# Performance work log

Hardware: AMD Instinct MI355X
Metric: run time of the kernel (lower is better)

## Reference

```python
import jax, jax.numpy as jnp
import numpy as np


def toeplitz_from(weight_matrix):
    # Faithful to the torch Toeplitz parametrization:
    # parameters = concat(W[::-1, 0], W[0, 1:]); toep[i, j] = parameters[n_rows-1-i+j]
    n_rows, n_cols = weight_matrix.shape
    params = jnp.concatenate([weight_matrix[::-1, 0], weight_matrix[0, 1:]])
    idx = (n_rows - 1) - jnp.arange(n_rows)[:, None] + jnp.arange(n_cols)[None, :]
    return params[idx]  # [n_rows, n_cols], built in one gather instead of a loop


def setup_inputs() -> dict:
    key = jax.random.key(0)
    ks = jax.random.split(key, 8)
    B, frame_dim, esn_dim, last_dim = 65536, 64, 960, 1024
    comb = frame_dim + esn_dim
    s1 = 1.0 / np.sqrt(comb)
    s2 = 1.0 / np.sqrt(last_dim)
    return {
        "x_frame": jax.random.normal(ks[0], (B, frame_dim), jnp.float32),
        "h_esn": jax.random.normal(ks[1], (B, esn_dim), jnp.float32),
        "W1": jax.random.normal(ks[2], (last_dim, comb), jnp.float32) * s1,
        "b1": jax.random.normal(ks[3], (last_dim,), jnp.float32) * s1,
        "W_slope": jax.random.normal(ks[4], (frame_dim, last_dim), jnp.float32) * s2,
        "b_slope": jax.random.normal(ks[5], (frame_dim,), jnp.float32) * s2,
        "W_int": jax.random.normal(ks[6], (frame_dim, last_dim), jnp.float32) * s2,
        "b_int": jax.random.normal(ks[7], (frame_dim,), jnp.float32) * s2,
    }


def reference(x_frame, h_esn, W1, b1, W_slope, b_slope, W_int, b_int):
    W1_toep = toeplitz_from(W1)                      # [last_dim, frame+esn]
    combined = jnp.concatenate([x_frame, h_esn], axis=-1)  # [B, frame+esn]
    q_last = jax.nn.relu(combined @ W1_toep.T + b1)  # [B, last_dim]
    slope = jnp.tanh(q_last @ W_slope.T + b_slope)   # [B, frame_dim]
    intercept = q_last @ W_int.T + b_int             # [B, frame_dim]
    return slope, intercept
```

## Files before the change

kernel.cpp:

```cpp
#include <hip/hip_runtime.h>
#include <cstdint>
#include <cstddef>

typedef __bf16 bf16x8v __attribute__((ext_vector_type(8)));
typedef float f32x4v __attribute__((ext_vector_type(4)));

__device__ __forceinline__ void gload_lds16(const void* g, void* l) {
  __builtin_amdgcn_global_load_lds((const __attribute__((address_space(1))) void*)g,
                                   (__attribute__((address_space(3))) void*)l,
                                   16, 0, 0);
}

__device__ __forceinline__ bf16x8v cvt_bf16x8(f32x4v a, f32x4v b) {
  bf16x8v r;
  r[0] = (__bf16)a[0]; r[1] = (__bf16)a[1]; r[2] = (__bf16)a[2]; r[3] = (__bf16)a[3];
  r[4] = (__bf16)b[0]; r[5] = (__bf16)b[1]; r[6] = (__bf16)b[2]; r[7] = (__bf16)b[3];
  return r;
}

__global__ __launch_bounds__(256) void prep_kernel(const float* __restrict__ W1,
                                                   const float* __restrict__ Wslope,
                                                   const float* __restrict__ Wint,
                                                   __bf16* __restrict__ toep,
                                                   __bf16* __restrict__ Wcat) {
  int id = blockIdx.x * 256 + threadIdx.x;
  if (id < 1024 * 1024) {
    int i = id >> 10, j = id & 1023;
    int p = 1023 - i + j;
    float v = (p < 1024) ? W1[(size_t)(1023 - p) << 10] : W1[p - 1023];
    toep[id] = (__bf16)v;
  } else {
    int id2 = id - 1024 * 1024;
    int n = id2 >> 10, k = id2 & 1023;
    float v = (n < 64) ? Wslope[((size_t)n << 10) + k] : Wint[((size_t)(n - 64) << 10) + k];
    Wcat[id2] = (__bf16)v;
  }
}

__global__ __launch_bounds__(256) void gemm1_f32dma(const float* __restrict__ x,
                                                    const float* __restrict__ h,
                                                    const __bf16* __restrict__ toep,
                                                    const float* __restrict__ b1,
                                                    __bf16* __restrict__ q) {
  __shared__ __align__(16) float  Af[2][128 * 32];
  __shared__ __align__(16) __bf16 Bf[2][128 * 32];
  const int tid = threadIdx.x, wid = tid >> 6, lane = tid & 63;
  const int wrow = wid >> 1, wcol = wid & 1;
  const int bid = blockIdx.x;
  const int xcd = bid & 7, j = bid >> 3;
  const int m0 = (((j >> 3) << 3) | xcd) << 7;
  const int n0 = (j & 7) << 7;
  const int quad = lane >> 4, l15 = lane & 15;
  const int rl8 = lane >> 3, s8 = lane & 7;
  const int sA = s8 ^ rl8;
  const int rl4 = lane >> 2, s4 = lane & 3;
  const int sB = s4 ^ (rl4 & 3);

  f32x4v acc[4][4] = {};

  const int arow = m0 + wid * 32;
  const __bf16* gB = toep + (((size_t)(n0 + wid * 32 + rl4)) << 10) + sB * 8;
  const size_t BROW16 = (size_t)16 << 10;

  auto stageA = [&](float* la, int kt) {
    const int k0 = kt << 5;
    const float* src;
    int rstride;
    if (k0 < 64) { src = x + (size_t)(arow + rl8) * 64 + k0 + sA * 4;        rstride = 8 * 64; }
    else         { src = h + (size_t)(arow + rl8) * 960 + (k0 - 64) + sA * 4; rstride = 8 * 960; }
    const int rb = wid * 32;
#pragma unroll
    for (int i = 0; i < 4; ++i) {
      gload_lds16(src, &la[(rb + i * 8) * 32]);
      src += rstride;
    }
  };
  auto stageB = [&](__bf16* lb) {
    const int rb = wid * 32;
    gload_lds16(gB,          &lb[rb * 32]);
    gload_lds16(gB + BROW16, &lb[(rb + 16) * 32]);
    gB += 32;
  };

  auto compute = [&](const float* la, const __bf16* lb) {
    bf16x8v af[4], bfr[4];
#pragma unroll
    for (int r = 0; r < 4; ++r) {
      const int row = wrow * 64 + r * 16 + l15;
      const f32x4v* base = (const f32x4v*)&la[row * 32];
      f32x4v lo = base[(quad * 2)     ^ (row & 7)];
      f32x4v hi = base[(quad * 2 + 1) ^ (row & 7)];
      af[r] = cvt_bf16x8(lo, hi);
    }
#pragma unroll
    for (int c = 0; c < 4; ++c) {
      const int row = wcol * 64 + c * 16 + l15;
      const bf16x8v* bb = (const bf16x8v*)&lb[row * 32];
      bfr[c] = bb[quad ^ (row & 3)];
    }
#pragma unroll
    for (int r = 0; r < 4; ++r)
#pragma unroll
      for (int c = 0; c < 4; ++c)
        acc[r][c] = __builtin_amdgcn_mfma_f32_16x16x32_bf16(af[r], bfr[c], acc[r][c], 0, 0, 0);
  };

  stageA(Af[0], 0); stageB(Bf[0]);
  for (int kt = 0; kt < 32; kt += 2) {
    __syncthreads();
    stageA(Af[1], kt + 1); stageB(Bf[1]);
    compute(Af[0], Bf[0]);
    __syncthreads();
    if (kt < 30) { stageA(Af[0], kt + 2); stageB(Bf[0]); }
    compute(Af[1], Bf[1]);
  }

#pragma unroll
  for (int c = 0; c < 4; ++c) {
    int col = n0 + wcol * 64 + c * 16 + l15;
    float bias = b1[col];
#pragma unroll
    for (int r = 0; r < 4; ++r)
#pragma unroll
      for (int e = 0; e < 4; ++e) {
        int row = m0 + wrow * 64 + r * 16 + quad * 4 + e;
        q[((size_t)row << 10) + col] = (__bf16)fmaxf(acc[r][c][e] + bias, 0.0f);
      }
  }
}

__global__ __launch_bounds__(256) void gemm2_dma(const __bf16* __restrict__ q,
                                                 const __bf16* __restrict__ Wcat,
                                                 const float* __restrict__ b_slope,
                                                 const float* __restrict__ b_int,
                                                 float* __restrict__ out) {
  __shared__ __align__(16) __bf16 Ab[2][64 * 64];
  __shared__ __align__(16) __bf16 Bb[2][128 * 64];
  const int tid = threadIdx.x, wid = tid >> 6, lane = tid & 63;
  const int wrow = wid >> 1, wcol = wid & 1;
  const int m0 = blockIdx.x << 6;
  const int quad = lane >> 4, l15 = lane & 15;
  const int r8 = lane >> 3, s8 = lane & 7;
  const int sw = (s8 ^ r8) * 8;

  f32x4v acc[2][4] = {};

  auto stage = [&](int buf, int kt) {
    int k0 = kt << 6;
#pragma unroll
    for (int j2 = 0; j2 < 2; ++j2) {
      int rb = wid * 16 + j2 * 8;
      gload_lds16(q + (((size_t)(m0 + rb + r8)) << 10) + k0 + sw, &Ab[buf][rb * 64]);
    }
#pragma unroll
    for (int j2 = 0; j2 < 4; ++j2) {
      int rb = wid * 32 + j2 * 8;
      gload_lds16(Wcat + (((size_t)(rb + r8)) << 10) + k0 + sw, &Bb[buf][rb * 64]);
    }
  };

  stage(0, 0);
  for (int kt = 0; kt < 16; ++kt) {
    int cur = kt & 1;
    __syncthreads();
    if (kt < 15) stage(cur ^ 1, kt + 1);
#pragma unroll
    for (int s = 0; s < 2; ++s) {
      bf16x8v af[2], bfr[4];
#pragma unroll
      for (int r = 0; r < 2; ++r) {
        const int row = wrow * 32 + r * 16 + l15;
        af[r] = *(const bf16x8v*)&Ab[cur][row * 64 + (((s * 4 + quad) ^ (row & 7)) * 8)];
      }
#pragma unroll
      for (int c = 0; c < 4; ++c) {
        const int row = wcol * 64 + c * 16 + l15;
        bfr[c] = *(const bf16x8v*)&Bb[cur][row * 64 + (((s * 4 + quad) ^ (row & 7)) * 8)];
      }
#pragma unroll
      for (int r = 0; r < 2; ++r)
#pragma unroll
        for (int c = 0; c < 4; ++c)
          acc[r][c] = __builtin_amdgcn_mfma_f32_16x16x32_bf16(af[r], bfr[c], acc[r][c], 0, 0, 0);
    }
  }

#pragma unroll
  for (int c = 0; c < 4; ++c) {
    int col = wcol * 64 + c * 16 + l15;
    float bias = (col < 64) ? b_slope[col] : b_int[col - 64];
#pragma unroll
    for (int r = 0; r < 2; ++r)
#pragma unroll
      for (int e = 0; e < 4; ++e) {
        int row = m0 + wrow * 32 + r * 16 + quad * 4 + e;
        float v = acc[r][c][e] + bias;
        if (col < 64) {
          float xc = fminf(fmaxf(v, -15.f), 15.f);
          float t = __expf(2.f * xc);
          out[(size_t)row * 64 + col] = (t - 1.f) / (t + 1.f);
        } else {
          out[(size_t)4194304 + (size_t)row * 64 + (col - 64)] = v;
        }
      }
  }
}

extern "C" void kernel_launch(void* const* d_in, const int* in_sizes, int n_in,
                              void* d_out, int out_size, void* d_ws, size_t ws_size,
                              hipStream_t stream) {
  const float* x  = (const float*)d_in[0];
  const float* h  = (const float*)d_in[1];
  const float* W1 = (const float*)d_in[2];
  const float* b1 = (const float*)d_in[3];
  const float* Ws = (const float*)d_in[4];
  const float* bs = (const float*)d_in[5];
  const float* Wi = (const float*)d_in[6];
  const float* bi = (const float*)d_in[7];
  char* ws = (char*)d_ws;

  const size_t SZ_Q    = 134217728;
  const size_t SZ_TOEP = 2097152;

  __bf16* q    = (__bf16*)ws;
  __bf16* toep = (__bf16*)(ws + SZ_Q);
  __bf16* Wcat = (__bf16*)(ws + SZ_Q + SZ_TOEP);

  hipLaunchKernelGGL(prep_kernel,  dim3(4608), dim3(256), 0, stream, W1, Ws, Wi, toep, Wcat);
  hipLaunchKernelGGL(gemm1_f32dma, dim3(4096), dim3(256), 0, stream, x, h, toep, b1, q);
  hipLaunchKernelGGL(gemm2_dma,    dim3(1024), dim3(256), 0, stream, q, Wcat, bs, bi,
                     (float*)d_out);
}
```

Before: 612.6 us.

## Convert A tiles to bf16 via registers and retile gemm2 to 128 rows

In gemm1, the fp32 activations are now loaded into registers one k-step ahead, converted to bf16 and written to LDS, replacing the direct fp32 DMA into LDS. This halves A's LDS footprint and removes per-compute conversions, at the cost of register pressure and a synchronous global-load path. The XOR swizzles are dropped, so LDS bank conflicts are possible. gemm2 now uses 128-row tiles with K steps of 32 and half as many blocks, trading occupancy for more reuse of Wcat per block.

```diff
diff --git a/kernel.cpp b/kernel.cpp
--- a/kernel.cpp
+++ b/kernel.cpp
@@ -37,13 +37,13 @@
   }
 }
 
-__global__ __launch_bounds__(256) void gemm1_f32dma(const float* __restrict__ x,
-                                                    const float* __restrict__ h,
-                                                    const __bf16* __restrict__ toep,
-                                                    const float* __restrict__ b1,
-                                                    __bf16* __restrict__ q) {
-  __shared__ __align__(16) float  Af[2][128 * 32];
-  __shared__ __align__(16) __bf16 Bf[2][128 * 32];
+__global__ __launch_bounds__(256) void gemm1_fused(const float* __restrict__ x,
+                                                   const float* __restrict__ h,
+                                                   const __bf16* __restrict__ toep,
+                                                   const float* __restrict__ b1,
+                                                   __bf16* __restrict__ q) {
+  __shared__ __align__(16) __bf16 Ab[2][128 * 32];
+  __shared__ __align__(16) __bf16 Bb[2][128 * 32];
   const int tid = threadIdx.x, wid = tid >> 6, lane = tid & 63;
   const int wrow = wid >> 1, wcol = wid & 1;
   const int bid = blockIdx.x;
@@ -51,53 +51,45 @@
   const int m0 = (((j >> 3) << 3) | xcd) << 7;
   const int n0 = (j & 7) << 7;
   const int quad = lane >> 4, l15 = lane & 15;
-  const int rl8 = lane >> 3, s8 = lane & 7;
-  const int sA = s8 ^ rl8;
-  const int rl4 = lane >> 2, s4 = lane & 3;
-  const int sB = s4 ^ (rl4 & 3);
+  const int rl = lane >> 2, seg = lane & 3;
 
   f32x4v acc[4][4] = {};
+  f32x4v rA[4];
 
   const int arow = m0 + wid * 32;
-  const __bf16* gB = toep + (((size_t)(n0 + wid * 32 + rl4)) << 10) + sB * 8;
-  const size_t BROW16 = (size_t)16 << 10;
-
-  auto stageA = [&](float* la, int kt) {
+  const __bf16* gB = toep + (((size_t)(n0 + wid * 32 + rl)) << 10) + seg * 8;
+  const size_t ROW16 = (size_t)16 << 10;
+
+  auto loadA = [&](int kt) {
     const int k0 = kt << 5;
-    const float* src;
-    int rstride;
-    if (k0 < 64) { src = x + (size_t)(arow + rl8) * 64 + k0 + sA * 4;        rstride = 8 * 64; }
-    else         { src = h + (size_t)(arow + rl8) * 960 + (k0 - 64) + sA * 4; rstride = 8 * 960; }
-    const int rb = wid * 32;
-#pragma unroll
-    for (int i = 0; i < 4; ++i) {
-      gload_lds16(src, &la[(rb + i * 8) * 32]);
-      src += rstride;
-    }
+    const float* src; size_t ld;
+    if (k0 < 64) { src = x + k0;      ld = 64;  }
+    else         { src = h + k0 - 64; ld = 960; }
+    const float* p0 = src + (size_t)(arow + rl) * ld + seg * 8;
+    const float* p1 = src + (size_t)(arow + rl + 16) * ld + seg * 8;
+    rA[0] = *(const f32x4v*)p0; rA[1] = *(const f32x4v*)(p0 + 4);
+    rA[2] = *(const f32x4v*)p1; rA[3] = *(const f32x4v*)(p1 + 4);
+  };
+  auto writeA = [&](__bf16* la) {
+    const int r0 = wid * 32 + rl;
+    *(bf16x8v*)&la[r0 * 32 + seg * 8]        = cvt_bf16x8(rA[0], rA[1]);
+    *(bf16x8v*)&la[(r0 + 16) * 32 + seg * 8] = cvt_bf16x8(rA[2], rA[3]);
   };
   auto stageB = [&](__bf16* lb) {
     const int rb = wid * 32;
-    gload_lds16(gB,          &lb[rb * 32]);
-    gload_lds16(gB + BROW16, &lb[(rb + 16) * 32]);
+    gload_lds16(gB,         &lb[rb * 32]);
+    gload_lds16(gB + ROW16, &lb[(rb + 16) * 32]);
     gB += 32;
   };
 
-  auto compute = [&](const float* la, const __bf16* lb) {
+  auto compute = [&](const __bf16* la, const __bf16* lb) {
     bf16x8v af[4], bfr[4];
 #pragma unroll
-    for (int r = 0; r < 4; ++r) {
-      const int row = wrow * 64 + r * 16 + l15;
-      const f32x4v* base = (const f32x4v*)&la[row * 32];
-      f32x4v lo = base[(quad * 2)     ^ (row & 7)];
-      f32x4v hi = base[(quad * 2 + 1) ^ (row & 7)];
-      af[r] = cvt_bf16x8(lo, hi);
-    }
-#pragma unroll
-    for (int c = 0; c < 4; ++c) {
-      const int row = wcol * 64 + c * 16 + l15;
-      const bf16x8v* bb = (const bf16x8v*)&lb[row * 32];
-      bfr[c] = bb[quad ^ (row & 3)];
-    }
+    for (int r = 0; r < 4; ++r)
+      af[r] = *(const bf16x8v*)&la[(wrow * 64 + r * 16 + l15) * 32 + quad * 8];
+#pragma unroll
+    for (int c = 0; c < 4; ++c)
+      bfr[c] = *(const bf16x8v*)&lb[(wcol * 64 + c * 16 + l15) * 32 + quad * 8];
 #pragma unroll
     for (int r = 0; r < 4; ++r)
 #pragma unroll
@@ -105,14 +97,20 @@
         acc[r][c] = __builtin_amdgcn_mfma_f32_16x16x32_bf16(af[r], bfr[c], acc[r][c], 0, 0, 0);
   };
 
-  stageA(Af[0], 0); stageB(Bf[0]);
-  for (int kt = 0; kt < 32; kt += 2) {
+  loadA(0);
+  stageB(Bb[0]);
+  writeA(Ab[0]);
+  loadA(1);
+
+  for (int kt = 0; kt < 32; ++kt) {
+    const int cur = kt & 1;
     __syncthreads();
-    stageA(Af[1], kt + 1); stageB(Bf[1]);
-    compute(Af[0], Bf[0]);
-    __syncthreads();
-    if (kt < 30) { stageA(Af[0], kt + 2); stageB(Bf[0]); }
-    compute(Af[1], Bf[1]);
+    if (kt < 31) {
+      stageB(Bb[cur ^ 1]);
+      writeA(Ab[cur ^ 1]);
+      if (kt < 30) loadA(kt + 2);
+    }
+    compute(Ab[cur], Bb[cur]);
   }
 
 #pragma unroll
@@ -129,60 +127,57 @@
   }
 }
 
-__global__ __launch_bounds__(256) void gemm2_dma(const __bf16* __restrict__ q,
-                                                 const __bf16* __restrict__ Wcat,
-                                                 const float* __restrict__ b_slope,
-                                                 const float* __restrict__ b_int,
-                                                 float* __restrict__ out) {
-  __shared__ __align__(16) __bf16 Ab[2][64 * 64];
-  __shared__ __align__(16) __bf16 Bb[2][128 * 64];
+__global__ __launch_bounds__(256) void gemm2_v2(const __bf16* __restrict__ q,
+                                                const __bf16* __restrict__ Wcat,
+                                                const float* __restrict__ b_slope,
+                                                const float* __restrict__ b_int,
+                                                float* __restrict__ out) {
+  __shared__ __align__(16) __bf16 Ab0[128 * 32], Ab1[128 * 32];
+  __shared__ __align__(16) __bf16 Bb0[128 * 32], Bb1[128 * 32];
   const int tid = threadIdx.x, wid = tid >> 6, lane = tid & 63;
   const int wrow = wid >> 1, wcol = wid & 1;
-  const int m0 = blockIdx.x << 6;
+  const int m0 = blockIdx.x << 7;
   const int quad = lane >> 4, l15 = lane & 15;
-  const int r8 = lane >> 3, s8 = lane & 7;
-  const int sw = (s8 ^ r8) * 8;
-
-  f32x4v acc[2][4] = {};
-
-  auto stage = [&](int buf, int kt) {
-    int k0 = kt << 6;
-#pragma unroll
-    for (int j2 = 0; j2 < 2; ++j2) {
-      int rb = wid * 16 + j2 * 8;
-      gload_lds16(q + (((size_t)(m0 + rb + r8)) << 10) + k0 + sw, &Ab[buf][rb * 64]);
-    }
-#pragma unroll
-    for (int j2 = 0; j2 < 4; ++j2) {
-      int rb = wid * 32 + j2 * 8;
-      gload_lds16(Wcat + (((size_t)(rb + r8)) << 10) + k0 + sw, &Bb[buf][rb * 64]);
-    }
-  };
-
-  stage(0, 0);
-  for (int kt = 0; kt < 16; ++kt) {
-    int cur = kt & 1;
+  const int rl = lane >> 2, seg = lane & 3;
+
+  f32x4v acc[4][4] = {};
+
+  const __bf16* gA = q    + (((size_t)(m0 + wid * 32 + rl)) << 10) + seg * 8;
+  const __bf16* gB = Wcat + (((size_t)(wid * 32 + rl)) << 10) + seg * 8;
+  const size_t ROW16 = (size_t)16 << 10;
+
+  auto stage = [&](__bf16* la, __bf16* lb) {
+    int rb = wid * 32;
+    gload_lds16(gA,         &la[rb * 32]);
+    gload_lds16(gA + ROW16, &la[(rb + 16) * 32]);
+    gload_lds16(gB,         &lb[rb * 32]);
+    gload_lds16(gB + ROW16, &lb[(rb + 16) * 32]);
+    gA += 32; gB += 32;
+  };
+
+  auto compute = [&](const __bf16* la, const __bf16* lb) {
+    bf16x8v af[4], bfr[4];
+#pragma unroll
+    for (int r = 0; r < 4; ++r)
+      af[r] = *(const bf16x8v*)&la[(wrow * 64 + r * 16 + l15) * 32 + quad * 8];
+#pragma unroll
+    for (int c = 0; c < 4; ++c)
+      bfr[c] = *(const bf16x8v*)&lb[(wcol * 64 + c * 16 + l15) * 32 + quad * 8];
+#pragma unroll
+    for (int r = 0; r < 4; ++r)
+#pragma unroll
+      for (int c = 0; c < 4; ++c)
+        acc[r][c] = __builtin_amdgcn_mfma_f32_16x16x32_bf16(af[r], bfr[c], acc[r][c], 0, 0, 0);
+  };
+
+  stage(Ab0, Bb0);
+  for (int kt = 0; kt < 32; kt += 2) {
     __syncthreads();
-    if (kt < 15) stage(cur ^ 1, kt + 1);
-#pragma unroll
-    for (int s = 0; s < 2; ++s) {
-      bf16x8v af[2], bfr[4];
-#pragma unroll
-      for (int r = 0; r < 2; ++r) {
-        const int row = wrow * 32 + r * 16 + l15;
-        af[r] = *(const bf16x8v*)&Ab[cur][row * 64 + (((s * 4 + quad) ^ (row & 7)) * 8)];
-      }
-#pragma unroll
-      for (int c = 0; c < 4; ++c) {
-        const int row = wcol * 64 + c * 16 + l15;
-        bfr[c] = *(const bf16x8v*)&Bb[cur][row * 64 + (((s * 4 + quad) ^ (row & 7)) * 8)];
-      }
-#pragma unroll
-      for (int r = 0; r < 2; ++r)
-#pragma unroll
-        for (int c = 0; c < 4; ++c)
-          acc[r][c] = __builtin_amdgcn_mfma_f32_16x16x32_bf16(af[r], bfr[c], acc[r][c], 0, 0, 0);
-    }
+    stage(Ab1, Bb1);
+    compute(Ab0, Bb0);
+    __syncthreads();
+    if (kt < 30) stage(Ab0, Bb0);
+    compute(Ab1, Bb1);
   }
 
 #pragma unroll
@@ -190,10 +185,10 @@
     int col = wcol * 64 + c * 16 + l15;
     float bias = (col < 64) ? b_slope[col] : b_int[col - 64];
 #pragma unroll
-    for (int r = 0; r < 2; ++r)
+    for (int r = 0; r < 4; ++r)
 #pragma unroll
       for (int e = 0; e < 4; ++e) {
-        int row = m0 + wrow * 32 + r * 16 + quad * 4 + e;
+        int row = m0 + wrow * 64 + r * 16 + quad * 4 + e;
         float v = acc[r][c][e] + bias;
         if (col < 64) {
           float xc = fminf(fmaxf(v, -15.f), 15.f);
@@ -226,8 +221,8 @@
   __bf16* toep = (__bf16*)(ws + SZ_Q);
   __bf16* Wcat = (__bf16*)(ws + SZ_Q + SZ_TOEP);
 
-  hipLaunchKernelGGL(prep_kernel,  dim3(4608), dim3(256), 0, stream, W1, Ws, Wi, toep, Wcat);
-  hipLaunchKernelGGL(gemm1_f32dma, dim3(4096), dim3(256), 0, stream, x, h, toep, b1, q);
-  hipLaunchKernelGGL(gemm2_dma,    dim3(1024), dim3(256), 0, stream, q, Wcat, bs, bi,
+  hipLaunchKernelGGL(prep_kernel, dim3(4608), dim3(256), 0, stream, W1, Ws, Wi, toep, Wcat);
+  hipLaunchKernelGGL(gemm1_fused, dim3(4096), dim3(256), 0, stream, x, h, toep, b1, q);
+  hipLaunchKernelGGL(gemm2_v2,    dim3(512),  dim3(256), 0, stream, q, Wcat, bs, bi,
                      (float*)d_out);
 }
```

Measured after the change: 602.8 us. About the same (-1.6%).
